# Performance work log

Measured on AMD Instinct MI355X. Metric: run time of the kernel, lower is better.

The kernel has to match this reference:

```python
import jax, jax.numpy as jnp
import numpy as np

N, F_IN, H, HEADS = 50000, 128, 128, 4
C = H // HEADS
E = 800000


def layer_norm(x, w, b, eps=1e-5):
    mu = x.mean(-1, keepdims=True)
    var = ((x - mu) ** 2).mean(-1, keepdims=True)
    return (x - mu) * jax.lax.rsqrt(var + eps) * w + b


def gat_conv(x, src, dst, edge_attr, W, att_src, att_dst, W_edge, att_edge, bias):
    """PyG GATConv (concat=True, add_self_loops=True, fill_value='mean', edge_dim=H), eval mode."""
    n = x.shape[0]
    # self-loop edge_attr = mean of incoming edge attrs per node (PyG fill_value='mean')
    ones = jnp.ones((src.shape[0],), dtype=edge_attr.dtype)
    deg = jax.ops.segment_sum(ones, dst, n)
    loop_attr = jax.ops.segment_sum(edge_attr, dst, n) / jnp.maximum(deg, 1.0)[:, None]
    loop = jnp.arange(n, dtype=src.dtype)
    src = jnp.concatenate([src, loop])
    dst = jnp.concatenate([dst, loop])
    ea = jnp.concatenate([edge_attr, loop_attr], axis=0)  # [E+N, H]
    h = (x @ W).reshape(n, HEADS, C)                      # [N, heads, C]
    a_src = (h * att_src).sum(-1)                         # [N, heads]
    a_dst = (h * att_dst).sum(-1)
    e = (ea @ W_edge).reshape(-1, HEADS, C)
    a_edge = (e * att_edge).sum(-1)                       # [E+N, heads]
    alpha = jax.nn.leaky_relu(a_src[src] + a_dst[dst] + a_edge, 0.2)
    # segment softmax over destination neighborhoods
    m = jax.lax.stop_gradient(jax.ops.segment_max(alpha, dst, n))
    alpha = jnp.exp(alpha - m[dst])
    s = jax.ops.segment_sum(alpha, dst, n)
    alpha = alpha / (s[dst] + 1e-16)
    out = jax.ops.segment_sum(alpha[:, :, None] * h[src], dst, n)  # [N, heads, C]
    return out.reshape(n, H) + bias


def setup_inputs() -> dict:
    key = jax.random.key(0)
    ks = iter(jax.random.split(key, 40))
    def lin(k, i, o, s=0.05):
        return jax.random.normal(k, (i, o), jnp.float32) * s
    d = {}
    d["x"] = jax.random.normal(next(ks), (N, F_IN), jnp.float32)
    d["edge_time"] = jax.random.uniform(next(ks), (E,), jnp.float32)
    d["ip_w1"] = lin(next(ks), F_IN, 2 * H); d["ip_b1"] = jnp.zeros((2 * H,), jnp.float32)
    d["ip_ln_w"] = jnp.ones((2 * H,), jnp.float32); d["ip_ln_b"] = jnp.zeros((2 * H,), jnp.float32)
    d["ip_w2"] = lin(next(ks), 2 * H, H); d["ip_b2"] = jnp.zeros((H,), jnp.float32)
    d["pn_w"] = jnp.ones((H,), jnp.float32); d["pn_b"] = jnp.zeros((H,), jnp.float32)
    d["ta_w1"] = lin(next(ks), 1, H); d["ta_b1"] = jnp.zeros((H,), jnp.float32)
    d["ta_ln_w"] = jnp.ones((H,), jnp.float32); d["ta_ln_b"] = jnp.zeros((H,), jnp.float32)
    d["ta_w2"] = lin(next(ks), H, H); d["ta_b2"] = jnp.zeros((H,), jnp.float32)
    for p in ("g1", "g2"):
        d[p + "_w"] = lin(next(ks), H, H)
        d[p + "_att_src"] = jax.random.normal(next(ks), (HEADS, C), jnp.float32) * 0.05
        d[p + "_att_dst"] = jax.random.normal(next(ks), (HEADS, C), jnp.float32) * 0.05
        d[p + "_ew"] = lin(next(ks), H, H)
        d[p + "_att_edge"] = jax.random.normal(next(ks), (HEADS, C), jnp.float32) * 0.05
        d[p + "_b"] = jnp.zeros((H,), jnp.float32)
    d["n1_w"] = jnp.ones((H,), jnp.float32); d["n1_b"] = jnp.zeros((H,), jnp.float32)
    d["n2_w"] = jnp.ones((H,), jnp.float32); d["n2_b"] = jnp.zeros((H,), jnp.float32)
    d["edge_index"] = jax.random.randint(next(ks), (2, E), 0, N, jnp.int32)
    return d


def reference(x, edge_time, ip_w1, ip_b1, ip_ln_w, ip_ln_b, ip_w2, ip_b2, pn_w, pn_b,
              ta_w1, ta_b1, ta_ln_w, ta_ln_b, ta_w2, ta_b2,
              g1_w, g1_att_src, g1_att_dst, g1_ew, g1_att_edge, g1_b,
              g2_w, g2_att_src, g2_att_dst, g2_ew, g2_att_edge, g2_b,
              n1_w, n1_b, n2_w, n2_b, edge_index):
    src, dst = edge_index[0], edge_index[1]
    # input projection: Linear -> ReLU -> LayerNorm -> (Dropout eval) -> Linear
    h = jax.nn.relu(x @ ip_w1 + ip_b1)
    h = layer_norm(h, ip_ln_w, ip_ln_b)
    h = h @ ip_w2 + ip_b2
    h = jnp.clip(jax.nn.relu(layer_norm(h, pn_w, pn_b)), -10.0, 10.0)
    # temporal attention MLP on edge times -> per-edge edge_attr [E, H]
    tw = edge_time[:, None] @ ta_w1 + ta_b1
    tw = jax.nn.relu(layer_norm(tw, ta_ln_w, ta_ln_b))
    tw = jnp.clip(jnp.tanh(tw @ ta_w2 + ta_b2), -3.0, 3.0)
    # GAT layer 1 (single chunk => residual + clamp, mean over 1 chunk is identity)
    g = gat_conv(h, src, dst, tw, g1_w, g1_att_src, g1_att_dst, g1_ew, g1_att_edge, g1_b) + h
    g = jax.nn.elu(layer_norm(jnp.clip(g, -10.0, 10.0), n1_w, n1_b))
    # GAT layer 2
    g2 = gat_conv(g, src, dst, tw, g2_w, g2_att_src, g2_att_dst, g2_ew, g2_att_edge, g2_b) + g
    return jax.nn.elu(layer_norm(jnp.clip(g2, -10.0, 10.0), n2_w, n2_b))
```

## Files before the change

### kernel.cpp

```cpp
#include <hip/hip_runtime.h>

typedef unsigned short u16;
typedef __attribute__((ext_vector_type(8))) short bf8_t;
typedef __attribute__((ext_vector_type(4))) float f4_t;

constexpr int NN   = 50000;
constexpr int NE   = 800000;
constexpr int TBLN = 2048;
constexpr int MB   = (NN + 31) / 32;
constexpr int FB   = NE / 256;

__device__ __forceinline__ float bf(const u16* p, int i) {
  return __uint_as_float(((unsigned)p[i]) << 16);
}
__device__ __forceinline__ u16 f2b(float f) {
  unsigned u = __float_as_uint(f);
  unsigned r = u + 0x7fffu + ((u >> 16) & 1u);
  return (u16)(r >> 16);
}
__device__ __forceinline__ short f2bs(float f) {
  unsigned u = __float_as_uint(f);
  unsigned r = u + 0x7fffu + ((u >> 16) & 1u);
  return (short)(r >> 16);
}
__device__ __forceinline__ u16 f2h(float f) {
  _Float16 h = (_Float16)f;
  return __builtin_bit_cast(unsigned short, h);
}
__device__ __forceinline__ float h2f(u16 v) {
  _Float16 h = __builtin_bit_cast(_Float16, v);
  return (float)h;
}
__device__ __forceinline__ unsigned packh(float a, float b) {
  return (unsigned)f2h(a) | ((unsigned)f2h(b) << 16);
}
__device__ __forceinline__ float blo(unsigned u) { return __uint_as_float(u << 16); }
__device__ __forceinline__ float bhi(unsigned u) { return __uint_as_float(u & 0xffff0000u); }
__device__ __forceinline__ float wred64(float v) {
#pragma unroll
  for (int o = 32; o; o >>= 1) v += __shfl_xor(v, o);
  return v;
}
__device__ __forceinline__ bf8_t ldv(const u16* p) { return *(const bf8_t*)p; }
__device__ __forceinline__ bf8_t ldcvt(const float* p) {
  const float4 a = *(const float4*)p;
  const float4 b = *(const float4*)(p + 4);
  bf8_t r;
  r[0] = f2bs(a.x); r[1] = f2bs(a.y); r[2] = f2bs(a.z); r[3] = f2bs(a.w);
  r[4] = f2bs(b.x); r[5] = f2bs(b.y); r[6] = f2bs(b.z); r[7] = f2bs(b.w);
  return r;
}
__device__ __forceinline__ f4_t mfma16(bf8_t a, bf8_t b, f4_t c) {
  return __builtin_amdgcn_mfma_f32_16x16x32_bf16(a, b, c, 0, 0, 0);
}

__global__ __launch_bounds__(256) void prep_k(
    const float* __restrict__ ew1, const float* __restrict__ ate1,
    const float* __restrict__ ew2, const float* __restrict__ ate2,
    float* __restrict__ V,
    const float* __restrict__ w1, const float* __restrict__ w2,
    const float* __restrict__ gw1, const float* __restrict__ gw2,
    u16* __restrict__ w1t, u16* __restrict__ w2t,
    u16* __restrict__ g1wt, u16* __restrict__ g2wt,
    const int* __restrict__ dstv, int* __restrict__ deg) {
  const int bid = blockIdx.x, t = threadIdx.x;
  if (bid == 0) {
#pragma unroll
    for (int rep = 0; rep < 2; ++rep) {
      int idx = t + rep * 256;
      int k = idx >> 2, hd = idx & 3;
      float s1 = 0.f, s2 = 0.f;
      for (int c = 0; c < 32; ++c) {
        s1 += ew1[k * 128 + hd * 32 + c] * ate1[hd * 32 + c];
        s2 += ew2[k * 128 + hd * 32 + c] * ate2[hd * 32 + c];
      }
      V[k * 8 + hd] = s1;
      V[k * 8 + 4 + hd] = s2;
    }
  } else if (bid <= 384) {
    int idx = (bid - 1) * 256 + t;
    if (idx < 32768) {
      int r = idx >> 8, c = idx & 255;
      w1t[c * 128 + r] = f2b(w1[idx]);
    } else if (idx < 65536) {
      int k = idx - 32768;
      int r = k >> 7, c = k & 127;
      w2t[c * 256 + r] = f2b(w2[k]);
    } else if (idx < 81920) {
      int k = idx - 65536;
      int r = k >> 7, c = k & 127;
      g1wt[c * 128 + r] = f2b(gw1[k]);
    } else {
      int k = idx - 81920;
      int r = k >> 7, c = k & 127;
      g2wt[c * 128 + r] = f2b(gw2[k]);
    }
  } else {
    int e = (bid - 385) * 256 + t;
    if (e < NE) atomicAdd(&deg[dstv[e]], 1);
  }
}

__global__ __launch_bounds__(128) void build_table(
    const float* __restrict__ taw1, const float* __restrict__ tab1,
    const float* __restrict__ talnw, const float* __restrict__ talnb,
    const float* __restrict__ taw2, const float* __restrict__ tab2,
    const float* __restrict__ V, float* __restrict__ tbl) {
  const int j = threadIdx.x;
  const int wv = j >> 6, ln = j & 63;
  const float t = (float)blockIdx.x / (float)(TBLN - 1);
  __shared__ float part[4];
  __shared__ float ush[128];
  __shared__ float pacc[16];
  float v = t * taw1[j] + tab1[j];
  float s = wred64(v), sq = wred64(v * v);
  if (ln == 0) { part[wv * 2] = s; part[wv * 2 + 1] = sq; }
  __syncthreads();
  float S = part[0] + part[2], SQ = part[1] + part[3];
  float mu = S * (1.f / 128.f);
  float var = SQ * (1.f / 128.f) - mu * mu;
  float rstd = rsqrtf(var + 1e-5f);
  float u = fmaxf((v - mu) * rstd * talnw[j] + talnb[j], 0.f);
  ush[j] = u;
  __syncthreads();
  float acc = 0.f;
  for (int k = 0; k < 128; ++k) acc += ush[k] * taw2[k * 128 + j];
  float w = tanhf(acc + tab2[j]);
  w = fminf(fmaxf(w, -3.f), 3.f);
#pragma unroll
  for (int p = 0; p < 8; ++p) {
    float z = wred64(w * V[j * 8 + p]);
    if (ln == 0) pacc[wv * 8 + p] = z;
  }
  __syncthreads();
  if (j < 8) tbl[blockIdx.x * 8 + j] = pacc[j] + pacc[8 + j];
}

__global__ __launch_bounds__(512) void scan1(const int* __restrict__ deg,
                                             int* __restrict__ indptr,
                                             int* __restrict__ blks) {
  const int t = threadIdx.x;
  const int i = blockIdx.x * 512 + t;
  int v = (i < NN) ? deg[i] : 0;
  const int lane = t & 63, wv = t >> 6;
  int x = v;
#pragma unroll
  for (int o = 1; o < 64; o <<= 1) {
    int y = __shfl_up(x, o);
    if (lane >= o) x += y;
  }
  __shared__ int ws[8];
  if (lane == 63) ws[wv] = x;
  __syncthreads();
  if (t < 8) {
    int y = ws[t];
#pragma unroll
    for (int o = 1; o < 8; o <<= 1) {
      int z = __shfl_up(y, o);
      if (t >= o) y += z;
    }
    ws[t] = y;
  }
  __syncthreads();
  int excl = wv ? ws[wv - 1] : 0;
  x += excl;
  if (i < NN) indptr[i + 1] = x;
  if (t == 511) blks[blockIdx.x] = x;
}
__global__ void scan2(int* __restrict__ blks, int nb) {
  const int t = threadIdx.x;
  int v = (t < nb) ? blks[t] : 0;
  const int lane = t & 63, wv = t >> 6;
  int x = v;
#pragma unroll
  for (int o = 1; o < 64; o <<= 1) {
    int y = __shfl_up(x, o);
    if (lane >= o) x += y;
  }
  __shared__ int ws[2];
  if (lane == 63) ws[wv] = x;
  __syncthreads();
  if (wv == 1) x += ws[0];
  if (t < nb) blks[t] = x - v;
}
__global__ __launch_bounds__(512) void scan3(int* __restrict__ indptr,
                                             const int* __restrict__ blks) {
  const int i = blockIdx.x * 512 + threadIdx.x;
  if (i < NN) indptr[i + 1] += blks[blockIdx.x];
  if (i == 0) indptr[0] = 0;
}

__device__ void fill_body(int fb, const int* __restrict__ srcv,
                          const int* __restrict__ dstv,
                          const float* __restrict__ etime,
                          const float* __restrict__ tbl,
                          const int* __restrict__ indptr, int* __restrict__ cursor,
                          u16* __restrict__ recs) {
  const int e = fb * 256 + threadIdx.x;
  if (e >= NE) return;
  int d = dstv[e];
  int p = atomicAdd(&cursor[d], 1);
  int pos = indptr[d] + p;
  float t = etime[e];
  t = fminf(fmaxf(t, 0.f), 1.f);
  float fpos = t * (float)(TBLN - 1);
  int i0 = (int)fpos;
  if (i0 > TBLN - 2) i0 = TBLN - 2;
  float fr = fpos - (float)i0;
  const float4* r = (const float4*)(tbl + i0 * 8);
  float4 a0 = r[0], a1 = r[1], b0 = r[2], b1 = r[3];
  float4 o1, o2;
  o1.x = a0.x + fr * (b0.x - a0.x); o1.y = a0.y + fr * (b0.y - a0.y);
  o1.z = a0.z + fr * (b0.z - a0.z); o1.w = a0.w + fr * (b0.w - a0.w);
  o2.x = a1.x + fr * (b1.x - a1.x); o2.y = a1.y + fr * (b1.y - a1.y);
  o2.z = a1.z + fr * (b1.z - a1.z); o2.w = a1.w + fr * (b1.w - a1.w);
  u16* rp = recs + (size_t)pos * 16;
  uint4 w;
  w.x = (unsigned)srcv[e];
  w.y = packh(o1.x, o1.y);
  w.z = packh(o1.z, o1.w);
  w.w = packh(o2.x, o2.y);
  *(uint4*)rp = w;
  *(unsigned*)(rp + 8) = packh(o2.z, o2.w);
}

__device__ void ip_body(int ipb, char* smem,
                        const float* __restrict__ x, const u16* __restrict__ w1t,
                        const float* __restrict__ b1, const float* __restrict__ ln1w,
                        const float* __restrict__ ln1b, const u16* __restrict__ w2t,
                        const float* __restrict__ b2, const float* __restrict__ pnw,
                        const float* __restrict__ pnb, u16* __restrict__ h16) {
  u16* h1n = (u16*)smem;
  u16* h2n = h1n;
  float* partS = (float*)(smem + 16896);
  float* partQ = (float*)(smem + 16896 + 512);

  const int t = threadIdx.x;
  const int w = t >> 6, lane = t & 63, q = lane >> 4, l15 = lane & 15;
  const int rowbase = ipb * 32;

  f4_t acc[2][4];
#pragma unroll
  for (int mt = 0; mt < 2; ++mt)
#pragma unroll
    for (int nt = 0; nt < 4; ++nt) acc[mt][nt] = (f4_t){0.f, 0.f, 0.f, 0.f};
#pragma unroll
  for (int kst = 0; kst < 4; ++kst) {
    int k0 = kst * 32 + q * 8;
    int r0 = rowbase + l15;      if (r0 > NN - 1) r0 = NN - 1;
    int r1 = rowbase + 16 + l15; if (r1 > NN - 1) r1 = NN - 1;
    bf8_t a0 = ldcvt(x + r0 * 128 + k0);
    bf8_t a1 = ldcvt(x + r1 * 128 + k0);
#pragma unroll
    for (int nt = 0; nt < 4; ++nt) {
      int n = w * 64 + nt * 16 + l15;
      bf8_t b = ldv(w1t + n * 128 + k0);
      acc[0][nt] = mfma16(a0, b, acc[0][nt]);
      acc[1][nt] = mfma16(a1, b, acc[1][nt]);
    }
  }
#pragma unroll
  for (int nt = 0; nt < 4; ++nt) {
    float bb = b1[w * 64 + nt * 16 + l15];
#pragma unroll
    for (int mt = 0; mt < 2; ++mt)
#pragma unroll
      for (int r = 0; r < 4; ++r)
        acc[mt][nt][r] = fmaxf(acc[mt][nt][r] + bb, 0.f);
  }
  {
    float s[2][4], sq[2][4];
#pragma unroll
    for (int mt = 0; mt < 2; ++mt)
#pragma unroll
      for (int r = 0; r < 4; ++r) {
        float a = acc[mt][0][r], b = acc[mt][1][r], c = acc[mt][2][r], d = acc[mt][3][r];
        s[mt][r] = a + b + c + d;
        sq[mt][r] = a * a + b * b + c * c + d * d;
      }
#pragma unroll
    for (int o = 1; o < 16; o <<= 1)
#pragma unroll
      for (int mt = 0; mt < 2; ++mt)
#pragma unroll
        for (int r = 0; r < 4; ++r) {
          s[mt][r] += __shfl_xor(s[mt][r], o);
          sq[mt][r] += __shfl_xor(sq[mt][r], o);
        }
    if (l15 == 0) {
#pragma unroll
      for (int mt = 0; mt < 2; ++mt)
#pragma unroll
        for (int r = 0; r < 4; ++r) {
          int row = mt * 16 + q * 4 + r;
          partS[w * 32 + row] = s[mt][r];
          partQ[w * 32 + row] = sq[mt][r];
        }
    }
  }
  __syncthreads();
  {
    float lw[4], lb[4];
#pragma unroll
    for (int nt = 0; nt < 4; ++nt) {
      int col = w * 64 + nt * 16 + l15;
      lw[nt] = ln1w[col]; lb[nt] = ln1b[col];
    }
#pragma unroll
    for (int mt = 0; mt < 2; ++mt)
#pragma unroll
      for (int r = 0; r < 4; ++r) {
        int row = mt * 16 + q * 4 + r;
        float S = partS[row] + partS[32 + row] + partS[64 + row] + partS[96 + row];
        float Q = partQ[row] + partQ[32 + row] + partQ[64 + row] + partQ[96 + row];
        float mu = S * (1.f / 256.f);
        float var = Q * (1.f / 256.f) - mu * mu;
        float rstd = rsqrtf(var + 1e-5f);
#pragma unroll
        for (int nt = 0; nt < 4; ++nt) {
          int col = w * 64 + nt * 16 + l15;
          h1n[row * 264 + col] = f2b((acc[mt][nt][r] - mu) * rstd * lw[nt] + lb[nt]);
        }
      }
  }
  __syncthreads();
  f4_t acc2[2][2];
#pragma unroll
  for (int mt = 0; mt < 2; ++mt)
#pragma unroll
    for (int nt = 0; nt < 2; ++nt) acc2[mt][nt] = (f4_t){0.f, 0.f, 0.f, 0.f};
#pragma unroll
  for (int kst = 0; kst < 8; ++kst) {
    int k0 = kst * 32 + q * 8;
    bf8_t a0 = ldv(h1n + (l15) * 264 + k0);
    bf8_t a1 = ldv(h1n + (16 + l15) * 264 + k0);
#pragma unroll
    for (int nt = 0; nt < 2; ++nt) {
      int n = w * 32 + nt * 16 + l15;
      bf8_t b = ldv(w2t + n * 256 + k0);
      acc2[0][nt] = mfma16(a0, b, acc2[0][nt]);
      acc2[1][nt] = mfma16(a1, b, acc2[1][nt]);
    }
  }
#pragma unroll
  for (int nt = 0; nt < 2; ++nt) {
    float bb = b2[w * 32 + nt * 16 + l15];
#pragma unroll
    for (int mt = 0; mt < 2; ++mt)
#pragma unroll
      for (int r = 0; r < 4; ++r)
        acc2[mt][nt][r] += bb;
  }
  {
    float s[2][4], sq[2][4];
#pragma unroll
    for (int mt = 0; mt < 2; ++mt)
#pragma unroll
      for (int r = 0; r < 4; ++r) {
        float a = acc2[mt][0][r], b = acc2[mt][1][r];
        s[mt][r] = a + b;
        sq[mt][r] = a * a + b * b;
      }
#pragma unroll
    for (int o = 1; o < 16; o <<= 1)
#pragma unroll
      for (int mt = 0; mt < 2; ++mt)
#pragma unroll
        for (int r = 0; r < 4; ++r) {
          s[mt][r] += __shfl_xor(s[mt][r], o);
          sq[mt][r] += __shfl_xor(sq[mt][r], o);
        }
    __syncthreads();
    if (l15 == 0) {
#pragma unroll
      for (int mt = 0; mt < 2; ++mt)
#pragma unroll
        for (int r = 0; r < 4; ++r) {
          int row = mt * 16 + q * 4 + r;
          partS[w * 32 + row] = s[mt][r];
          partQ[w * 32 + row] = sq[mt][r];
        }
    }
  }
  __syncthreads();
  {
    float lw[2], lb[2];
#pragma unroll
    for (int nt = 0; nt < 2; ++nt) {
      int col = w * 32 + nt * 16 + l15;
      lw[nt] = pnw[col]; lb[nt] = pnb[col];
    }
#pragma unroll
    for (int mt = 0; mt < 2; ++mt)
#pragma unroll
      for (int r = 0; r < 4; ++r) {
        int row = mt * 16 + q * 4 + r;
        float S = partS[row] + partS[32 + row] + partS[64 + row] + partS[96 + row];
        float Q = partQ[row] + partQ[32 + row] + partQ[64 + row] + partQ[96 + row];
        float mu = S * (1.f / 128.f);
        float var = Q * (1.f / 128.f) - mu * mu;
        float rstd = rsqrtf(var + 1e-5f);
#pragma unroll
        for (int nt = 0; nt < 2; ++nt) {
          int col = w * 32 + nt * 16 + l15;
          float v = (acc2[mt][nt][r] - mu) * rstd * lw[nt] + lb[nt];
          v = fminf(fmaxf(v, 0.f), 10.f);
          h2n[row * 128 + col] = f2b(v);
        }
      }
  }
  __syncthreads();
  {
    const int row = t >> 3, cb = (t & 7) * 16;
    int rg = rowbase + row;
    if (rg < NN) {
      uint4 v0 = *(const uint4*)(h2n + row * 128 + cb);
      uint4 v1 = *(const uint4*)(h2n + row * 128 + cb + 8);
      *(uint4*)(h16 + rg * 128 + cb) = v0;
      *(uint4*)(h16 + rg * 128 + cb + 8) = v1;
    }
  }
}

__global__ __launch_bounds__(256) void fillip_k(
    const int* srcv, const int* dstv, const float* etime, const float* tbl,
    const int* indptr, int* cursor, u16* recs,
    const float* x, const u16* w1t, const float* b1, const float* ln1w,
    const float* ln1b, const u16* w2t, const float* b2, const float* pnw,
    const float* pnb, u16* h16) {
  __shared__ char smem[17920];
  const int bid = blockIdx.x;
  if (bid % 3 == 0) {
    ip_body(bid / 3, smem, x, w1t, b1, ln1w, ln1b, w2t, b2, pnw, pnb, h16);
  } else {
    fill_body(bid - bid / 3 - 1, srcv, dstv, etime, tbl, indptr, cursor, recs);
  }
}

__global__ __launch_bounds__(256) void hp_mfma(
    const u16* __restrict__ feat16, const u16* __restrict__ wt,
    const float* __restrict__ attsrc, const float* __restrict__ attdst,
    u16* __restrict__ hp16, float* __restrict__ asrc, float* __restrict__ adst) {
  const int t = threadIdx.x;
  const int w = t >> 6, lane = t & 63, q = lane >> 4, l15 = lane & 15;
  const int rowbase = blockIdx.x * 32;
  f4_t acc[2][2];
#pragma unroll
  for (int mt = 0; mt < 2; ++mt)
#pragma unroll
    for (int nt = 0; nt < 2; ++nt) acc[mt][nt] = (f4_t){0.f, 0.f, 0.f, 0.f};
#pragma unroll
  for (int kst = 0; kst < 4; ++kst) {
    int k0 = kst * 32 + q * 8;
    int r0 = rowbase + l15;      if (r0 > NN - 1) r0 = NN - 1;
    int r1 = rowbase + 16 + l15; if (r1 > NN - 1) r1 = NN - 1;
    bf8_t a0 = ldv(feat16 + r0 * 128 + k0);
    bf8_t a1 = ldv(feat16 + r1 * 128 + k0);
#pragma unroll
    for (int nt = 0; nt < 2; ++nt) {
      int n = w * 32 + nt * 16 + l15;
      bf8_t b = ldv(wt + n * 128 + k0);
      acc[0][nt] = mfma16(a0, b, acc[0][nt]);
      acc[1][nt] = mfma16(a1, b, acc[1][nt]);
    }
  }
  float ps[2][4], pd[2][4];
#pragma unroll
  for (int mt = 0; mt < 2; ++mt)
#pragma unroll
    for (int r = 0; r < 4; ++r) { ps[mt][r] = 0.f; pd[mt][r] = 0.f; }
#pragma unroll
  for (int mt = 0; mt < 2; ++mt)
#pragma unroll
    for (int nt = 0; nt < 2; ++nt) {
      int col = w * 32 + nt * 16 + l15;
      float as = attsrc[col], ad = attdst[col];
#pragma unroll
      for (int r = 0; r < 4; ++r) {
        int row = mt * 16 + q * 4 + r;
        int rg = rowbase + row;
        float v = acc[mt][nt][r];
        if (rg < NN) hp16[(size_t)rg * 128 + col] = f2b(v);
        ps[mt][r] += v * as;
        pd[mt][r] += v * ad;
      }
    }
#pragma unroll
  for (int o = 1; o < 16; o <<= 1)
#pragma unroll
    for (int mt = 0; mt < 2; ++mt)
#pragma unroll
      for (int r = 0; r < 4; ++r) {
        ps[mt][r] += __shfl_xor(ps[mt][r], o);
        pd[mt][r] += __shfl_xor(pd[mt][r], o);
      }
  if (l15 == 0) {
#pragma unroll
    for (int mt = 0; mt < 2; ++mt)
#pragma unroll
      for (int r = 0; r < 4; ++r) {
        int rg = rowbase + mt * 16 + q * 4 + r;
        if (rg < NN) {
          asrc[rg * 4 + w] = ps[mt][r];
          adst[rg * 4 + w] = pd[mt][r];
        }
      }
  }
}

template <int L, int FINAL>
__global__ __launch_bounds__(256) void agg_k(
    const int* __restrict__ indptr, const u16* __restrict__ recs,
    const float* __restrict__ asrc, const float* __restrict__ adst,
    const u16* __restrict__ hp16, const u16* __restrict__ feat16,
    const float* __restrict__ gbias, const float* __restrict__ lnw,
    const float* __restrict__ lnb, u16* __restrict__ gout16,
    float* __restrict__ out32) {
  const int wv = threadIdx.x >> 6, lane = threadIdx.x & 63;
  const int n = blockIdx.x * 4 + wv;
  if (n >= NN) return;
  const int s0 = indptr[n], s1 = indptr[n + 1];
  const int dg = s1 - s0;
  const int g = lane >> 4, sl = lane & 15, cb = sl * 8, hdB = sl >> 2;
  const float advB = adst[n * 4 + hdB];
  float ssp = 0.f, sap = 0.f;
  float acc[8];
#pragma unroll
  for (int i = 0; i < 8; ++i) acc[i] = 0.f;
  for (int base = s0; base < s1; base += 8) {
    int i0 = base + g, i1 = base + 4 + g;
    int j0 = i0 < s1 ? i0 : s1 - 1;
    int j1 = i1 < s1 ? i1 : s1 - 1;
    const u16* r0 = recs + (size_t)j0 * 16;
    const u16* r1 = recs + (size_t)j1 * 16;
    int sc0 = *(const int*)r0, sc1 = *(const int*)r1;
    float ae0 = h2f(r0[2 + 4 * L + hdB]);
    float ae1v = h2f(r1[2 + 4 * L + hdB]);
    float as0 = asrc[sc0 * 4 + hdB], as1 = asrc[sc1 * 4 + hdB];
    const uint4 row0 = *(const uint4*)(hp16 + (size_t)sc0 * 128 + cb);
    const uint4 row1 = *(const uint4*)(hp16 + (size_t)sc1 * 128 + cb);
    float l0 = as0 + advB + ae0; l0 = fmaxf(l0, 0.2f * l0);
    float l1 = as1 + advB + ae1v; l1 = fmaxf(l1, 0.2f * l1);
    float w0 = (i0 < s1) ? __expf(l0) : 0.f;
    float w1 = (i1 < s1) ? __expf(l1) : 0.f;
    ssp += w0 + w1;
    sap += ((i0 < s1) ? ae0 : 0.f) + ((i1 < s1) ? ae1v : 0.f);
    acc[0] += w0 * blo(row0.x) + w1 * blo(row1.x);
    acc[1] += w0 * bhi(row0.x) + w1 * bhi(row1.x);
    acc[2] += w0 * blo(row0.y) + w1 * blo(row1.y);
    acc[3] += w0 * bhi(row0.y) + w1 * bhi(row1.y);
    acc[4] += w0 * blo(row0.z) + w1 * blo(row1.z);
    acc[5] += w0 * bhi(row0.z) + w1 * bhi(row1.z);
    acc[6] += w0 * blo(row0.w) + w1 * blo(row1.w);
    acc[7] += w0 * bhi(row0.w) + w1 * bhi(row1.w);
  }
#pragma unroll
  for (int i = 0; i < 8; ++i) {
    acc[i] += __shfl_xor(acc[i], 16);
    acc[i] += __shfl_xor(acc[i], 32);
  }
  ssp += __shfl_xor(ssp, 16); ssp += __shfl_xor(ssp, 32);
  sap += __shfl_xor(sap, 16); sap += __shfl_xor(sap, 32);
  const float degf = (float)(dg > 0 ? dg : 1);
  float asnB = asrc[n * 4 + hdB];
  float la = asnB + advB + sap / degf;
  la = fmaxf(la, 0.2f * la);
  float wsf = __expf(la);
  float inv = 1.f / (ssp + wsf + 1e-16f);
  const uint4 rs4 = *(const uint4*)(hp16 + (size_t)n * 128 + cb);
  const uint4 rr4 = *(const uint4*)(feat16 + (size_t)n * 128 + cb);
  const float4 gb0 = *(const float4*)(gbias + cb);
  const float4 gb1 = *(const float4*)(gbias + cb + 4);
  float v[8];
  v[0] = (acc[0] + wsf * blo(rs4.x)) * inv + gb0.x + blo(rr4.x);
  v[1] = (acc[1] + wsf * bhi(rs4.x)) * inv + gb0.y + bhi(rr4.x);
  v[2] = (acc[2] + wsf * blo(rs4.y)) * inv + gb0.z + blo(rr4.y);
  v[3] = (acc[3] + wsf * bhi(rs4.y)) * inv + gb0.w + bhi(rr4.y);
  v[4] = (acc[4] + wsf * blo(rs4.z)) * inv + gb1.x + blo(rr4.z);
  v[5] = (acc[5] + wsf * bhi(rs4.z)) * inv + gb1.y + bhi(rr4.z);
  v[6] = (acc[6] + wsf * blo(rs4.w)) * inv + gb1.z + blo(rr4.w);
  v[7] = (acc[7] + wsf * bhi(rs4.w)) * inv + gb1.w + bhi(rr4.w);
  float sum = 0.f, sq = 0.f;
#pragma unroll
  for (int i = 0; i < 8; ++i) {
    v[i] = fminf(fmaxf(v[i], -10.f), 10.f);
    sum += v[i]; sq += v[i] * v[i];
  }
#pragma unroll
  for (int o = 1; o < 16; o <<= 1) {
    sum += __shfl_xor(sum, o);
    sq += __shfl_xor(sq, o);
  }
  float mu = sum * (1.f / 128.f);
  float var = sq * (1.f / 128.f) - mu * mu;
  float rstd = rsqrtf(var + 1e-5f);
  const float4 lw0 = *(const float4*)(lnw + cb);
  const float4 lw1 = *(const float4*)(lnw + cb + 4);
  const float4 lb0 = *(const float4*)(lnb + cb);
  const float4 lb1 = *(const float4*)(lnb + cb + 4);
  float y[8];
  y[0] = (v[0] - mu) * rstd * lw0.x + lb0.x;
  y[1] = (v[1] - mu) * rstd * lw0.y + lb0.y;
  y[2] = (v[2] - mu) * rstd * lw0.z + lb0.z;
  y[3] = (v[3] - mu) * rstd * lw0.w + lb0.w;
  y[4] = (v[4] - mu) * rstd * lw1.x + lb1.x;
  y[5] = (v[5] - mu) * rstd * lw1.y + lb1.y;
  y[6] = (v[6] - mu) * rstd * lw1.z + lb1.z;
  y[7] = (v[7] - mu) * rstd * lw1.w + lb1.w;
#pragma unroll
  for (int i = 0; i < 8; ++i) y[i] = y[i] > 0.f ? y[i] : expm1f(y[i]);
  if (g == 0) {
    if (FINAL) {
      float4 o0 = {y[0], y[1], y[2], y[3]};
      float4 o1 = {y[4], y[5], y[6], y[7]};
      *(float4*)(out32 + (size_t)n * 128 + cb) = o0;
      *(float4*)(out32 + (size_t)n * 128 + cb + 4) = o1;
    } else {
      uint4 o;
      o.x = (unsigned)f2b(y[0]) | ((unsigned)f2b(y[1]) << 16);
      o.y = (unsigned)f2b(y[2]) | ((unsigned)f2b(y[3]) << 16);
      o.z = (unsigned)f2b(y[4]) | ((unsigned)f2b(y[5]) << 16);
      o.w = (unsigned)f2b(y[6]) | ((unsigned)f2b(y[7]) << 16);
      *(uint4*)(gout16 + (size_t)n * 128 + cb) = o;
    }
  }
}

extern "C" void kernel_launch(void* const* d_in, const int* in_sizes, int n_in,
                              void* d_out, int out_size, void* d_ws, size_t ws_size,
                              hipStream_t stream) {
  const float* x      = (const float*)d_in[0];
  const float* etime  = (const float*)d_in[1];
  const float* ip_w1  = (const float*)d_in[2];
  const float* ip_b1  = (const float*)d_in[3];
  const float* ip_lnw = (const float*)d_in[4];
  const float* ip_lnb = (const float*)d_in[5];
  const float* ip_w2  = (const float*)d_in[6];
  const float* ip_b2  = (const float*)d_in[7];
  const float* pn_w   = (const float*)d_in[8];
  const float* pn_b   = (const float*)d_in[9];
  const float* ta_w1  = (const float*)d_in[10];
  const float* ta_b1  = (const float*)d_in[11];
  const float* ta_lnw = (const float*)d_in[12];
  const float* ta_lnb = (const float*)d_in[13];
  const float* ta_w2  = (const float*)d_in[14];
  const float* ta_b2  = (const float*)d_in[15];
  const float* g1_w   = (const float*)d_in[16];
  const float* g1_as  = (const float*)d_in[17];
  const float* g1_ad  = (const float*)d_in[18];
  const float* g1_ew  = (const float*)d_in[19];
  const float* g1_ae  = (const float*)d_in[20];
  const float* g1_b   = (const float*)d_in[21];
  const float* g2_w   = (const float*)d_in[22];
  const float* g2_as  = (const float*)d_in[23];
  const float* g2_ad  = (const float*)d_in[24];
  const float* g2_ew  = (const float*)d_in[25];
  const float* g2_ae  = (const float*)d_in[26];
  const float* g2_b   = (const float*)d_in[27];
  const float* n1_w   = (const float*)d_in[28];
  const float* n1_b   = (const float*)d_in[29];
  const float* n2_w   = (const float*)d_in[30];
  const float* n2_b   = (const float*)d_in[31];
  const int* eidx     = (const int*)d_in[32];
  const int* srcv = eidx;
  const int* dstv = eidx + NE;

  char* p = (char*)d_ws;
  auto carve = [&](size_t bytes) -> char* {
    char* r = p;
    p += (bytes + 255) & ~(size_t)255;
    return r;
  };
  u16*   h16    = (u16*)carve((size_t)NN * 128 * 2);
  u16*   g16    = (u16*)carve((size_t)NN * 128 * 2);
  u16*   hp16   = (u16*)carve((size_t)NN * 128 * 2);
  float* asrc   = (float*)carve((size_t)NN * 4 * 4);
  float* adst   = (float*)carve((size_t)NN * 4 * 4);
  u16*   recs   = (u16*)carve((size_t)NE * 32);
  int*   deg    = (int*)carve((size_t)NN * 4);
  int*   indptr = (int*)carve((size_t)(NN + 1) * 4);
  int*   cursor = (int*)carve((size_t)NN * 4);
  int*   blks   = (int*)carve(512 * 4);
  float* V      = (float*)carve(128 * 8 * 4);
  float* tbl    = (float*)carve((size_t)TBLN * 8 * 4);
  u16*   w1t    = (u16*)carve(128 * 256 * 2);
  u16*   w2t    = (u16*)carve(256 * 128 * 2);
  u16*   g1wt   = (u16*)carve(128 * 128 * 2);
  u16*   g2wt   = (u16*)carve(128 * 128 * 2);

  hipMemsetAsync(deg, 0, (size_t)NN * 4, stream);
  hipMemsetAsync(cursor, 0, (size_t)NN * 4, stream);

  const int SCB = (NN + 511) / 512;

  prep_k<<<1 + 384 + FB, 256, 0, stream>>>(g1_ew, g1_ae, g2_ew, g2_ae, V,
                                           ip_w1, ip_w2, g1_w, g2_w,
                                           w1t, w2t, g1wt, g2wt, dstv, deg);
  build_table<<<TBLN, 128, 0, stream>>>(ta_w1, ta_b1, ta_lnw, ta_lnb, ta_w2, ta_b2, V, tbl);
  scan1<<<SCB, 512, 0, stream>>>(deg, indptr, blks);
  scan2<<<1, 128, 0, stream>>>(blks, SCB);
  scan3<<<SCB, 512, 0, stream>>>(indptr, blks);
  fillip_k<<<MB + FB, 256, 0, stream>>>(srcv, dstv, etime, tbl, indptr, cursor, recs,
                                        x, w1t, ip_b1, ip_lnw, ip_lnb, w2t, ip_b2,
                                        pn_w, pn_b, h16);
  hp_mfma<<<MB, 256, 0, stream>>>(h16, g1wt, g1_as, g1_ad, hp16, asrc, adst);
  agg_k<0, 0><<<NN / 4, 256, 0, stream>>>(indptr, recs, asrc, adst, hp16, h16,
                                          g1_b, n1_w, n1_b, g16, nullptr);
  hp_mfma<<<MB, 256, 0, stream>>>(g16, g2wt, g2_as, g2_ad, hp16, asrc, adst);
  agg_k<1, 1><<<NN / 4, 256, 0, stream>>>(indptr, recs, asrc, adst, hp16, g16,
                                          g2_b, n2_w, n2_b, nullptr, (float*)d_out);
}
```

Baseline: 394.1 us.

## Scatter compact edge records, then expand time attributes in a coalesced pass

The edge fill pass now scatters only an 8-byte (src, time) record per edge into CSR order, instead of a 32-byte record that included interpolated attention values. A new attrize pass, fused into the first hp_mfma launch via block-index partitioning, reads these compact records sequentially. It does the table interpolation and writes the full 32-byte records contiguously. scan3 now initializes cursor to each row's start offset, which removes the cursor memset and the indptr read during fill. The trade-off is an extra read and write pass over the edge records, and the compact buffer aliases g16, which relies on it being consumed before agg_k writes g16.

```diff
diff --git a/kernel.cpp b/kernel.cpp
--- a/kernel.cpp
+++ b/kernel.cpp
@@ -10,9 +10,6 @@
 constexpr int MB   = (NN + 31) / 32;
 constexpr int FB   = NE / 256;
 
-__device__ __forceinline__ float bf(const u16* p, int i) {
-  return __uint_as_float(((unsigned)p[i]) << 16);
-}
 __device__ __forceinline__ u16 f2b(float f) {
   unsigned u = __float_as_uint(f);
   unsigned r = u + 0x7fffu + ((u >> 16) & 1u);
@@ -184,44 +181,33 @@
   if (t < nb) blks[t] = x - v;
 }
 __global__ __launch_bounds__(512) void scan3(int* __restrict__ indptr,
-                                             const int* __restrict__ blks) {
+                                             const int* __restrict__ blks,
+                                             const int* __restrict__ deg,
+                                             int* __restrict__ cursor) {
   const int i = blockIdx.x * 512 + threadIdx.x;
-  if (i < NN) indptr[i + 1] += blks[blockIdx.x];
+  if (i < NN) {
+    int v = indptr[i + 1] + blks[blockIdx.x];
+    indptr[i + 1] = v;
+    cursor[i] = v - deg[i];
+  }
   if (i == 0) indptr[0] = 0;
 }
 
 __device__ void fill_body(int fb, const int* __restrict__ srcv,
                           const int* __restrict__ dstv,
                           const float* __restrict__ etime,
-                          const float* __restrict__ tbl,
-                          const int* __restrict__ indptr, int* __restrict__ cursor,
-                          u16* __restrict__ recs) {
+                          int* __restrict__ cursor,
+                          int2* __restrict__ rec8) {
   const int e = fb * 256 + threadIdx.x;
   if (e >= NE) return;
+  int s = srcv[e];
+  float t = etime[e];
   int d = dstv[e];
-  int p = atomicAdd(&cursor[d], 1);
-  int pos = indptr[d] + p;
-  float t = etime[e];
-  t = fminf(fmaxf(t, 0.f), 1.f);
-  float fpos = t * (float)(TBLN - 1);
-  int i0 = (int)fpos;
-  if (i0 > TBLN - 2) i0 = TBLN - 2;
-  float fr = fpos - (float)i0;
-  const float4* r = (const float4*)(tbl + i0 * 8);
-  float4 a0 = r[0], a1 = r[1], b0 = r[2], b1 = r[3];
-  float4 o1, o2;
-  o1.x = a0.x + fr * (b0.x - a0.x); o1.y = a0.y + fr * (b0.y - a0.y);
-  o1.z = a0.z + fr * (b0.z - a0.z); o1.w = a0.w + fr * (b0.w - a0.w);
-  o2.x = a1.x + fr * (b1.x - a1.x); o2.y = a1.y + fr * (b1.y - a1.y);
-  o2.z = a1.z + fr * (b1.z - a1.z); o2.w = a1.w + fr * (b1.w - a1.w);
-  u16* rp = recs + (size_t)pos * 16;
-  uint4 w;
-  w.x = (unsigned)srcv[e];
-  w.y = packh(o1.x, o1.y);
-  w.z = packh(o1.z, o1.w);
-  w.w = packh(o2.x, o2.y);
-  *(uint4*)rp = w;
-  *(unsigned*)(rp + 8) = packh(o2.z, o2.w);
+  int pos = atomicAdd(&cursor[d], 1);
+  int2 r;
+  r.x = s;
+  r.y = __float_as_int(t);
+  rec8[pos] = r;
 }
 
 __device__ void ip_body(int ipb, char* smem,
@@ -423,8 +409,8 @@
 }
 
 __global__ __launch_bounds__(256) void fillip_k(
-    const int* srcv, const int* dstv, const float* etime, const float* tbl,
-    const int* indptr, int* cursor, u16* recs,
+    const int* srcv, const int* dstv, const float* etime,
+    int* cursor, int2* rec8,
     const float* x, const u16* w1t, const float* b1, const float* ln1w,
     const float* ln1b, const u16* w2t, const float* b2, const float* pnw,
     const float* pnb, u16* h16) {
@@ -433,17 +419,61 @@
   if (bid % 3 == 0) {
     ip_body(bid / 3, smem, x, w1t, b1, ln1w, ln1b, w2t, b2, pnw, pnb, h16);
   } else {
-    fill_body(bid - bid / 3 - 1, srcv, dstv, etime, tbl, indptr, cursor, recs);
-  }
-}
-
+    fill_body(bid - bid / 3 - 1, srcv, dstv, etime, cursor, rec8);
+  }
+}
+
+__device__ void attrize_body(int ab, const int2* __restrict__ rec8,
+                             const float* __restrict__ tbl,
+                             u16* __restrict__ recs) {
+  const int e = ab * 256 + threadIdx.x;
+  if (e >= NE) return;
+  int2 r = rec8[e];
+  float t = __int_as_float(r.y);
+  t = fminf(fmaxf(t, 0.f), 1.f);
+  float fpos = t * (float)(TBLN - 1);
+  int i0 = (int)fpos;
+  if (i0 > TBLN - 2) i0 = TBLN - 2;
+  float fr = fpos - (float)i0;
+  const float4* rp4 = (const float4*)(tbl + i0 * 8);
+  float4 a0 = rp4[0], a1 = rp4[1], b0 = rp4[2], b1 = rp4[3];
+  float4 o1, o2;
+  o1.x = a0.x + fr * (b0.x - a0.x); o1.y = a0.y + fr * (b0.y - a0.y);
+  o1.z = a0.z + fr * (b0.z - a0.z); o1.w = a0.w + fr * (b0.w - a0.w);
+  o2.x = a1.x + fr * (b1.x - a1.x); o2.y = a1.y + fr * (b1.y - a1.y);
+  o2.z = a1.z + fr * (b1.z - a1.z); o2.w = a1.w + fr * (b1.w - a1.w);
+  u16* rp = recs + (size_t)e * 16;
+  uint4 w;
+  w.x = (unsigned)r.x;
+  w.y = packh(o1.x, o1.y);
+  w.z = packh(o1.z, o1.w);
+  w.w = packh(o2.x, o2.y);
+  *(uint4*)rp = w;
+  *(unsigned*)(rp + 8) = packh(o2.z, o2.w);
+}
+
+template <int WITH_ATTR>
 __global__ __launch_bounds__(256) void hp_mfma(
     const u16* __restrict__ feat16, const u16* __restrict__ wt,
     const float* __restrict__ attsrc, const float* __restrict__ attdst,
-    u16* __restrict__ hp16, float* __restrict__ asrc, float* __restrict__ adst) {
+    u16* __restrict__ hp16, float* __restrict__ asrc, float* __restrict__ adst,
+    const int2* __restrict__ rec8, const float* __restrict__ tbl,
+    u16* __restrict__ recs) {
+  int mb;
+  if (WITH_ATTR) {
+    const int bid = blockIdx.x;
+    if (bid % 3 != 0) {
+      attrize_body(bid - bid / 3 - 1, rec8, tbl, recs);
+      return;
+    }
+    mb = bid / 3;
+    if (mb >= MB) return;
+  } else {
+    mb = blockIdx.x;
+  }
   const int t = threadIdx.x;
   const int w = t >> 6, lane = t & 63, q = lane >> 4, l15 = lane & 15;
-  const int rowbase = blockIdx.x * 32;
+  const int rowbase = mb * 32;
   f4_t acc[2][2];
 #pragma unroll
   for (int mt = 0; mt < 2; ++mt)
@@ -687,9 +717,9 @@
   u16*   w2t    = (u16*)carve(256 * 128 * 2);
   u16*   g1wt   = (u16*)carve(128 * 128 * 2);
   u16*   g2wt   = (u16*)carve(128 * 128 * 2);
+  int2*  rec8   = (int2*)g16;
 
   hipMemsetAsync(deg, 0, (size_t)NN * 4, stream);
-  hipMemsetAsync(cursor, 0, (size_t)NN * 4, stream);
 
   const int SCB = (NN + 511) / 512;
 
@@ -699,14 +729,16 @@
   build_table<<<TBLN, 128, 0, stream>>>(ta_w1, ta_b1, ta_lnw, ta_lnb, ta_w2, ta_b2, V, tbl);
   scan1<<<SCB, 512, 0, stream>>>(deg, indptr, blks);
   scan2<<<1, 128, 0, stream>>>(blks, SCB);
-  scan3<<<SCB, 512, 0, stream>>>(indptr, blks);
-  fillip_k<<<MB + FB, 256, 0, stream>>>(srcv, dstv, etime, tbl, indptr, cursor, recs,
+  scan3<<<SCB, 512, 0, stream>>>(indptr, blks, deg, cursor);
+  fillip_k<<<MB + FB, 256, 0, stream>>>(srcv, dstv, etime, cursor, rec8,
                                         x, w1t, ip_b1, ip_lnw, ip_lnb, w2t, ip_b2,
                                         pn_w, pn_b, h16);
-  hp_mfma<<<MB, 256, 0, stream>>>(h16, g1wt, g1_as, g1_ad, hp16, asrc, adst);
+  hp_mfma<1><<<3 * MB, 256, 0, stream>>>(h16, g1wt, g1_as, g1_ad, hp16, asrc, adst,
+                                         rec8, tbl, recs);
   agg_k<0, 0><<<NN / 4, 256, 0, stream>>>(indptr, recs, asrc, adst, hp16, h16,
                                           g1_b, n1_w, n1_b, g16, nullptr);
-  hp_mfma<<<MB, 256, 0, stream>>>(g16, g2wt, g2_as, g2_ad, hp16, asrc, adst);
+  hp_mfma<0><<<MB, 256, 0, stream>>>(g16, g2wt, g2_as, g2_ad, hp16, asrc, adst,
+                                     rec8, tbl, recs);
   agg_k<1, 1><<<NN / 4, 256, 0, stream>>>(indptr, recs, asrc, adst, hp16, g16,
                                           g2_b, n2_w, n2_b, nullptr, (float*)d_out);
 }
```

Measured after the change: 403.6 us. +2.4%, slower.

## Enlarge GEMM row tiles to 64, pre-convert x to bf16, precompute edge cursors

Applied to the files above, without the earlier changes.

The input-projection and attention GEMM kernels now process 64 rows per block instead of 32, reusing each weight fragment across four M tiles. The input x is converted to bf16 in the prep kernel, stored in the not-yet-used g16 buffer, and loaded directly by the MLP. scan3 now seeds the per-node cursor with the absolute CSR start offset, which removes the cursor memset and the indptr lookup in the edge fill. The trade-offs are fewer blocks, which lowers parallelism, higher register and LDS use, and an extra conversion pass over x.

```diff
diff --git a/kernel.cpp b/kernel.cpp
--- a/kernel.cpp
+++ b/kernel.cpp
@@ -7,22 +7,14 @@
 constexpr int NN   = 50000;
 constexpr int NE   = 800000;
 constexpr int TBLN = 2048;
-constexpr int MB   = (NN + 31) / 32;
+constexpr int MB64 = (NN + 63) / 64;
 constexpr int FB   = NE / 256;
 
-__device__ __forceinline__ float bf(const u16* p, int i) {
-  return __uint_as_float(((unsigned)p[i]) << 16);
-}
 __device__ __forceinline__ u16 f2b(float f) {
   unsigned u = __float_as_uint(f);
   unsigned r = u + 0x7fffu + ((u >> 16) & 1u);
   return (u16)(r >> 16);
 }
-__device__ __forceinline__ short f2bs(float f) {
-  unsigned u = __float_as_uint(f);
-  unsigned r = u + 0x7fffu + ((u >> 16) & 1u);
-  return (short)(r >> 16);
-}
 __device__ __forceinline__ u16 f2h(float f) {
   _Float16 h = (_Float16)f;
   return __builtin_bit_cast(unsigned short, h);
@@ -42,14 +34,6 @@
   return v;
 }
 __device__ __forceinline__ bf8_t ldv(const u16* p) { return *(const bf8_t*)p; }
-__device__ __forceinline__ bf8_t ldcvt(const float* p) {
-  const float4 a = *(const float4*)p;
-  const float4 b = *(const float4*)(p + 4);
-  bf8_t r;
-  r[0] = f2bs(a.x); r[1] = f2bs(a.y); r[2] = f2bs(a.z); r[3] = f2bs(a.w);
-  r[4] = f2bs(b.x); r[5] = f2bs(b.y); r[6] = f2bs(b.z); r[7] = f2bs(b.w);
-  return r;
-}
 __device__ __forceinline__ f4_t mfma16(bf8_t a, bf8_t b, f4_t c) {
   return __builtin_amdgcn_mfma_f32_16x16x32_bf16(a, b, c, 0, 0, 0);
 }
@@ -62,7 +46,8 @@
     const float* __restrict__ gw1, const float* __restrict__ gw2,
     u16* __restrict__ w1t, u16* __restrict__ w2t,
     u16* __restrict__ g1wt, u16* __restrict__ g2wt,
-    const int* __restrict__ dstv, int* __restrict__ deg) {
+    const int* __restrict__ dstv, int* __restrict__ deg,
+    const float* __restrict__ x, u16* __restrict__ x16) {
   const int bid = blockIdx.x, t = threadIdx.x;
   if (bid == 0) {
 #pragma unroll
@@ -95,9 +80,20 @@
       int r = k >> 7, c = k & 127;
       g2wt[c * 128 + r] = f2b(gw2[k]);
     }
-  } else {
+  } else if (bid <= 384 + FB) {
     int e = (bid - 385) * 256 + t;
     if (e < NE) atomicAdd(&deg[dstv[e]], 1);
+  } else {
+    int idx = (bid - 385 - FB) * 256 + t;
+    size_t e8 = (size_t)idx * 8;
+    const float4 a = *(const float4*)(x + e8);
+    const float4 b = *(const float4*)(x + e8 + 4);
+    uint4 o;
+    o.x = (unsigned)f2b(a.x) | ((unsigned)f2b(a.y) << 16);
+    o.y = (unsigned)f2b(a.z) | ((unsigned)f2b(a.w) << 16);
+    o.z = (unsigned)f2b(b.x) | ((unsigned)f2b(b.y) << 16);
+    o.w = (unsigned)f2b(b.z) | ((unsigned)f2b(b.w) << 16);
+    *(uint4*)(x16 + e8) = o;
   }
 }
 
@@ -184,9 +180,15 @@
   if (t < nb) blks[t] = x - v;
 }
 __global__ __launch_bounds__(512) void scan3(int* __restrict__ indptr,
-                                             const int* __restrict__ blks) {
+                                             const int* __restrict__ blks,
+                                             const int* __restrict__ deg,
+                                             int* __restrict__ cursor) {
   const int i = blockIdx.x * 512 + threadIdx.x;
-  if (i < NN) indptr[i + 1] += blks[blockIdx.x];
+  if (i < NN) {
+    int v = indptr[i + 1] + blks[blockIdx.x];
+    indptr[i + 1] = v;
+    cursor[i] = v - deg[i];
+  }
   if (i == 0) indptr[0] = 0;
 }
 
@@ -194,13 +196,12 @@
                           const int* __restrict__ dstv,
                           const float* __restrict__ etime,
                           const float* __restrict__ tbl,
-                          const int* __restrict__ indptr, int* __restrict__ cursor,
+                          int* __restrict__ cursor,
                           u16* __restrict__ recs) {
   const int e = fb * 256 + threadIdx.x;
   if (e >= NE) return;
   int d = dstv[e];
-  int p = atomicAdd(&cursor[d], 1);
-  int pos = indptr[d] + p;
+  int pos = atomicAdd(&cursor[d], 1);
   float t = etime[e];
   t = fminf(fmaxf(t, 0.f), 1.f);
   float fpos = t * (float)(TBLN - 1);
@@ -225,63 +226,67 @@
 }
 
 __device__ void ip_body(int ipb, char* smem,
-                        const float* __restrict__ x, const u16* __restrict__ w1t,
+                        const u16* __restrict__ x16, const u16* __restrict__ w1t,
                         const float* __restrict__ b1, const float* __restrict__ ln1w,
                         const float* __restrict__ ln1b, const u16* __restrict__ w2t,
                         const float* __restrict__ b2, const float* __restrict__ pnw,
                         const float* __restrict__ pnb, u16* __restrict__ h16) {
   u16* h1n = (u16*)smem;
   u16* h2n = h1n;
-  float* partS = (float*)(smem + 16896);
-  float* partQ = (float*)(smem + 16896 + 512);
+  float* partS = (float*)(smem + 33792);
+  float* partQ = (float*)(smem + 33792 + 1024);
 
   const int t = threadIdx.x;
   const int w = t >> 6, lane = t & 63, q = lane >> 4, l15 = lane & 15;
-  const int rowbase = ipb * 32;
-
-  f4_t acc[2][4];
-#pragma unroll
-  for (int mt = 0; mt < 2; ++mt)
+  const int rowbase = ipb * 64;
+
+  f4_t acc[4][4];
+#pragma unroll
+  for (int mt = 0; mt < 4; ++mt)
 #pragma unroll
     for (int nt = 0; nt < 4; ++nt) acc[mt][nt] = (f4_t){0.f, 0.f, 0.f, 0.f};
 #pragma unroll
   for (int kst = 0; kst < 4; ++kst) {
     int k0 = kst * 32 + q * 8;
-    int r0 = rowbase + l15;      if (r0 > NN - 1) r0 = NN - 1;
-    int r1 = rowbase + 16 + l15; if (r1 > NN - 1) r1 = NN - 1;
-    bf8_t a0 = ldcvt(x + r0 * 128 + k0);
-    bf8_t a1 = ldcvt(x + r1 * 128 + k0);
+    bf8_t a[4];
+#pragma unroll
+    for (int mt = 0; mt < 4; ++mt) {
+      int r = rowbase + mt * 16 + l15;
+      if (r > NN - 1) r = NN - 1;
+      a[mt] = ldv(x16 + (size_t)r * 128 + k0);
+    }
 #pragma unroll
     for (int nt = 0; nt < 4; ++nt) {
       int n = w * 64 + nt * 16 + l15;
       bf8_t b = ldv(w1t + n * 128 + k0);
-      acc[0][nt] = mfma16(a0, b, acc[0][nt]);
-      acc[1][nt] = mfma16(a1, b, acc[1][nt]);
+#pragma unroll
+      for (int mt = 0; mt < 4; ++mt)
+        acc[mt][nt] = mfma16(a[mt], b, acc[mt][nt]);
     }
   }
 #pragma unroll
   for (int nt = 0; nt < 4; ++nt) {
     float bb = b1[w * 64 + nt * 16 + l15];
 #pragma unroll
-    for (int mt = 0; mt < 2; ++mt)
+    for (int mt = 0; mt < 4; ++mt)
 #pragma unroll
       for (int r = 0; r < 4; ++r)
         acc[mt][nt][r] = fmaxf(acc[mt][nt][r] + bb, 0.f);
   }
   {
-    float s[2][4], sq[2][4];
-#pragma unroll
-    for (int mt = 0; mt < 2; ++mt)
+    float s[4][4], sq[4][4];
+#pragma unroll
+    for (int mt = 0; mt < 4; ++mt)
 #pragma unroll
       for (int r = 0; r < 4; ++r) {
-        float a = acc[mt][0][r], b = acc[mt][1][r], c = acc[mt][2][r], d = acc[mt][3][r];
-        s[mt][r] = a + b + c + d;
-        sq[mt][r] = a * a + b * b + c * c + d * d;
+        float a0 = acc[mt][0][r], b0 = acc[mt][1][r], c0 = acc[mt][2][r], d0 = acc[mt][3][r];
+        s[mt][r] = a0 + b0 + c0 + d0;
+        sq[mt][r] = a0 * a0 + b0 * b0 + c0 * c0 + d0 * d0;
       }
 #pragma unroll
     for (int o = 1; o < 16; o <<= 1)
 #pragma unroll
-      for (int mt = 0; mt < 2; ++mt)
+      for (int mt = 0; mt < 4; ++mt)
 #pragma unroll
         for (int r = 0; r < 4; ++r) {
           s[mt][r] += __shfl_xor(s[mt][r], o);
@@ -289,12 +294,12 @@
         }
     if (l15 == 0) {
 #pragma unroll
-      for (int mt = 0; mt < 2; ++mt)
+      for (int mt = 0; mt < 4; ++mt)
 #pragma unroll
         for (int r = 0; r < 4; ++r) {
           int row = mt * 16 + q * 4 + r;
-          partS[w * 32 + row] = s[mt][r];
-          partQ[w * 32 + row] = sq[mt][r];
+          partS[w * 64 + row] = s[mt][r];
+          partQ[w * 64 + row] = sq[mt][r];
         }
     }
   }
@@ -307,12 +312,12 @@
       lw[nt] = ln1w[col]; lb[nt] = ln1b[col];
     }
 #pragma unroll
-    for (int mt = 0; mt < 2; ++mt)
+    for (int mt = 0; mt < 4; ++mt)
 #pragma unroll
       for (int r = 0; r < 4; ++r) {
         int row = mt * 16 + q * 4 + r;
-        float S = partS[row] + partS[32 + row] + partS[64 + row] + partS[96 + row];
-        float Q = partQ[row] + partQ[32 + row] + partQ[64 + row] + partQ[96 + row];
+        float S = partS[row] + partS[64 + row] + partS[128 + row] + partS[192 + row];
+        float Q = partQ[row] + partQ[64 + row] + partQ[128 + row] + partQ[192 + row];
         float mu = S * (1.f / 256.f);
         float var = Q * (1.f / 256.f) - mu * mu;
         float rstd = rsqrtf(var + 1e-5f);
@@ -324,47 +329,50 @@
       }
   }
   __syncthreads();
-  f4_t acc2[2][2];
-#pragma unroll
-  for (int mt = 0; mt < 2; ++mt)
+  f4_t acc2[4][2];
+#pragma unroll
+  for (int mt = 0; mt < 4; ++mt)
 #pragma unroll
     for (int nt = 0; nt < 2; ++nt) acc2[mt][nt] = (f4_t){0.f, 0.f, 0.f, 0.f};
 #pragma unroll
   for (int kst = 0; kst < 8; ++kst) {
     int k0 = kst * 32 + q * 8;
-    bf8_t a0 = ldv(h1n + (l15) * 264 + k0);
-    bf8_t a1 = ldv(h1n + (16 + l15) * 264 + k0);
+    bf8_t a[4];
+#pragma unroll
+    for (int mt = 0; mt < 4; ++mt)
+      a[mt] = ldv(h1n + (mt * 16 + l15) * 264 + k0);
 #pragma unroll
     for (int nt = 0; nt < 2; ++nt) {
       int n = w * 32 + nt * 16 + l15;
       bf8_t b = ldv(w2t + n * 256 + k0);
-      acc2[0][nt] = mfma16(a0, b, acc2[0][nt]);
-      acc2[1][nt] = mfma16(a1, b, acc2[1][nt]);
+#pragma unroll
+      for (int mt = 0; mt < 4; ++mt)
+        acc2[mt][nt] = mfma16(a[mt], b, acc2[mt][nt]);
     }
   }
 #pragma unroll
   for (int nt = 0; nt < 2; ++nt) {
     float bb = b2[w * 32 + nt * 16 + l15];
 #pragma unroll
-    for (int mt = 0; mt < 2; ++mt)
+    for (int mt = 0; mt < 4; ++mt)
 #pragma unroll
       for (int r = 0; r < 4; ++r)
         acc2[mt][nt][r] += bb;
   }
   {
-    float s[2][4], sq[2][4];
-#pragma unroll
-    for (int mt = 0; mt < 2; ++mt)
+    float s[4][4], sq[4][4];
+#pragma unroll
+    for (int mt = 0; mt < 4; ++mt)
 #pragma unroll
       for (int r = 0; r < 4; ++r) {
-        float a = acc2[mt][0][r], b = acc2[mt][1][r];
-        s[mt][r] = a + b;
-        sq[mt][r] = a * a + b * b;
+        float a0 = acc2[mt][0][r], b0 = acc2[mt][1][r];
+        s[mt][r] = a0 + b0;
+        sq[mt][r] = a0 * a0 + b0 * b0;
       }
 #pragma unroll
     for (int o = 1; o < 16; o <<= 1)
 #pragma unroll
-      for (int mt = 0; mt < 2; ++mt)
+      for (int mt = 0; mt < 4; ++mt)
 #pragma unroll
         for (int r = 0; r < 4; ++r) {
           s[mt][r] += __shfl_xor(s[mt][r], o);
@@ -373,12 +381,12 @@
     __syncthreads();
     if (l15 == 0) {
 #pragma unroll
-      for (int mt = 0; mt < 2; ++mt)
+      for (int mt = 0; mt < 4; ++mt)
 #pragma unroll
         for (int r = 0; r < 4; ++r) {
           int row = mt * 16 + q * 4 + r;
-          partS[w * 32 + row] = s[mt][r];
-          partQ[w * 32 + row] = sq[mt][r];
+          partS[w * 64 + row] = s[mt][r];
+          partQ[w * 64 + row] = sq[mt][r];
         }
     }
   }
@@ -391,12 +399,12 @@
       lw[nt] = pnw[col]; lb[nt] = pnb[col];
     }
 #pragma unroll
-    for (int mt = 0; mt < 2; ++mt)
+    for (int mt = 0; mt < 4; ++mt)
 #pragma unroll
       for (int r = 0; r < 4; ++r) {
         int row = mt * 16 + q * 4 + r;
-        float S = partS[row] + partS[32 + row] + partS[64 + row] + partS[96 + row];
-        float Q = partQ[row] + partQ[32 + row] + partQ[64 + row] + partQ[96 + row];
+        float S = partS[row] + partS[64 + row] + partS[128 + row] + partS[192 + row];
+        float Q = partQ[row] + partQ[64 + row] + partQ[128 + row] + partQ[192 + row];
         float mu = S * (1.f / 128.f);
         float var = Q * (1.f / 128.f) - mu * mu;
         float rstd = rsqrtf(var + 1e-5f);
@@ -411,29 +419,30 @@
   }
   __syncthreads();
   {
-    const int row = t >> 3, cb = (t & 7) * 16;
+    const int row = t >> 2, cb = (t & 3) * 32;
     int rg = rowbase + row;
     if (rg < NN) {
-      uint4 v0 = *(const uint4*)(h2n + row * 128 + cb);
-      uint4 v1 = *(const uint4*)(h2n + row * 128 + cb + 8);
-      *(uint4*)(h16 + rg * 128 + cb) = v0;
-      *(uint4*)(h16 + rg * 128 + cb + 8) = v1;
+#pragma unroll
+      for (int c = 0; c < 4; ++c) {
+        uint4 v0 = *(const uint4*)(h2n + row * 128 + cb + c * 8);
+        *(uint4*)(h16 + (size_t)rg * 128 + cb + c * 8) = v0;
+      }
     }
   }
 }
 
 __global__ __launch_bounds__(256) void fillip_k(
     const int* srcv, const int* dstv, const float* etime, const float* tbl,
-    const int* indptr, int* cursor, u16* recs,
-    const float* x, const u16* w1t, const float* b1, const float* ln1w,
+    int* cursor, u16* recs,
+    const u16* x16, const u16* w1t, const float* b1, const float* ln1w,
     const float* ln1b, const u16* w2t, const float* b2, const float* pnw,
     const float* pnb, u16* h16) {
-  __shared__ char smem[17920];
+  __shared__ char smem[35840];
   const int bid = blockIdx.x;
-  if (bid % 3 == 0) {
-    ip_body(bid / 3, smem, x, w1t, b1, ln1w, ln1b, w2t, b2, pnw, pnb, h16);
+  if (bid % 5 == 0) {
+    ip_body(bid / 5, smem, x16, w1t, b1, ln1w, ln1b, w2t, b2, pnw, pnb, h16);
   } else {
-    fill_body(bid - bid / 3 - 1, srcv, dstv, etime, tbl, indptr, cursor, recs);
+    fill_body(bid - bid / 5 - 1, srcv, dstv, etime, tbl, cursor, recs);
   }
 }
 
@@ -443,34 +452,38 @@
     u16* __restrict__ hp16, float* __restrict__ asrc, float* __restrict__ adst) {
   const int t = threadIdx.x;
   const int w = t >> 6, lane = t & 63, q = lane >> 4, l15 = lane & 15;
-  const int rowbase = blockIdx.x * 32;
-  f4_t acc[2][2];
-#pragma unroll
-  for (int mt = 0; mt < 2; ++mt)
+  const int rowbase = blockIdx.x * 64;
+  f4_t acc[4][2];
+#pragma unroll
+  for (int mt = 0; mt < 4; ++mt)
 #pragma unroll
     for (int nt = 0; nt < 2; ++nt) acc[mt][nt] = (f4_t){0.f, 0.f, 0.f, 0.f};
 #pragma unroll
   for (int kst = 0; kst < 4; ++kst) {
     int k0 = kst * 32 + q * 8;
-    int r0 = rowbase + l15;      if (r0 > NN - 1) r0 = NN - 1;
-    int r1 = rowbase + 16 + l15; if (r1 > NN - 1) r1 = NN - 1;
-    bf8_t a0 = ldv(feat16 + r0 * 128 + k0);
-    bf8_t a1 = ldv(feat16 + r1 * 128 + k0);
+    bf8_t a[4];
+#pragma unroll
+    for (int mt = 0; mt < 4; ++mt) {
+      int r = rowbase + mt * 16 + l15;
+      if (r > NN - 1) r = NN - 1;
+      a[mt] = ldv(feat16 + (size_t)r * 128 + k0);
+    }
 #pragma unroll
     for (int nt = 0; nt < 2; ++nt) {
       int n = w * 32 + nt * 16 + l15;
       bf8_t b = ldv(wt + n * 128 + k0);
-      acc[0][nt] = mfma16(a0, b, acc[0][nt]);
-      acc[1][nt] = mfma16(a1, b, acc[1][nt]);
-    }
-  }
-  float ps[2][4], pd[2][4];
-#pragma unroll
-  for (int mt = 0; mt < 2; ++mt)
+#pragma unroll
+      for (int mt = 0; mt < 4; ++mt)
+        acc[mt][nt] = mfma16(a[mt], b, acc[mt][nt]);
+    }
+  }
+  float ps[4][4], pd[4][4];
+#pragma unroll
+  for (int mt = 0; mt < 4; ++mt)
 #pragma unroll
     for (int r = 0; r < 4; ++r) { ps[mt][r] = 0.f; pd[mt][r] = 0.f; }
 #pragma unroll
-  for (int mt = 0; mt < 2; ++mt)
+  for (int mt = 0; mt < 4; ++mt)
 #pragma unroll
     for (int nt = 0; nt < 2; ++nt) {
       int col = w * 32 + nt * 16 + l15;
@@ -488,7 +501,7 @@
 #pragma unroll
   for (int o = 1; o < 16; o <<= 1)
 #pragma unroll
-    for (int mt = 0; mt < 2; ++mt)
+    for (int mt = 0; mt < 4; ++mt)
 #pragma unroll
       for (int r = 0; r < 4; ++r) {
         ps[mt][r] += __shfl_xor(ps[mt][r], o);
@@ -496,7 +509,7 @@
       }
   if (l15 == 0) {
 #pragma unroll
-    for (int mt = 0; mt < 2; ++mt)
+    for (int mt = 0; mt < 4; ++mt)
 #pragma unroll
       for (int r = 0; r < 4; ++r) {
         int rg = rowbase + mt * 16 + q * 4 + r;
@@ -687,26 +700,27 @@
   u16*   w2t    = (u16*)carve(256 * 128 * 2);
   u16*   g1wt   = (u16*)carve(128 * 128 * 2);
   u16*   g2wt   = (u16*)carve(128 * 128 * 2);
+  u16*   x16    = (u16*)g16;
 
   hipMemsetAsync(deg, 0, (size_t)NN * 4, stream);
-  hipMemsetAsync(cursor, 0, (size_t)NN * 4, stream);
 
   const int SCB = (NN + 511) / 512;
 
-  prep_k<<<1 + 384 + FB, 256, 0, stream>>>(g1_ew, g1_ae, g2_ew, g2_ae, V,
-                                           ip_w1, ip_w2, g1_w, g2_w,
-                                           w1t, w2t, g1wt, g2wt, dstv, deg);
+  prep_k<<<1 + 384 + FB + FB, 256, 0, stream>>>(g1_ew, g1_ae, g2_ew, g2_ae, V,
+                                                ip_w1, ip_w2, g1_w, g2_w,
+                                                w1t, w2t, g1wt, g2wt, dstv, deg,
+                                                x, x16);
   build_table<<<TBLN, 128, 0, stream>>>(ta_w1, ta_b1, ta_lnw, ta_lnb, ta_w2, ta_b2, V, tbl);
   scan1<<<SCB, 512, 0, stream>>>(deg, indptr, blks);
   scan2<<<1, 128, 0, stream>>>(blks, SCB);
-  scan3<<<SCB, 512, 0, stream>>>(indptr, blks);
-  fillip_k<<<MB + FB, 256, 0, stream>>>(srcv, dstv, etime, tbl, indptr, cursor, recs,
-                                        x, w1t, ip_b1, ip_lnw, ip_lnb, w2t, ip_b2,
-                                        pn_w, pn_b, h16);
-  hp_mfma<<<MB, 256, 0, stream>>>(h16, g1wt, g1_as, g1_ad, hp16, asrc, adst);
+  scan3<<<SCB, 512, 0, stream>>>(indptr, blks, deg, cursor);
+  fillip_k<<<MB64 + FB, 256, 0, stream>>>(srcv, dstv, etime, tbl, cursor, recs,
+                                          x16, w1t, ip_b1, ip_lnw, ip_lnb, w2t, ip_b2,
+                                          pn_w, pn_b, h16);
+  hp_mfma<<<MB64, 256, 0, stream>>>(h16, g1wt, g1_as, g1_ad, hp16, asrc, adst);
   agg_k<0, 0><<<NN / 4, 256, 0, stream>>>(indptr, recs, asrc, adst, hp16, h16,
                                           g1_b, n1_w, n1_b, g16, nullptr);
-  hp_mfma<<<MB, 256, 0, stream>>>(g16, g2wt, g2_as, g2_ad, hp16, asrc, adst);
+  hp_mfma<<<MB64, 256, 0, stream>>>(g16, g2wt, g2_as, g2_ad, hp16, asrc, adst);
   agg_k<1, 1><<<NN / 4, 256, 0, stream>>>(indptr, recs, asrc, adst, hp16, g16,
                                           g2_b, n2_w, n2_b, nullptr, (float*)d_out);
 }
```

Result: no change. 389.7 us (-1.1%).
